# Performance work log

Hardware: AMD Instinct MI355X
Metric: run time of the kernel (lower is better)

## Reference

```python
import jax, jax.numpy as jnp
import numpy as np

M = 8          # ensemble size
B = 16384      # batch
HIST = 5       # history
L = 384        # latent_dim
A = 1          # action_dim
HID = 512      # hidden_dim
NHL = 2        # num_hidden_layers
DIN = L * HIST + A * HIST  # 1925
EPS = 1e-5     # BatchNorm eps


def setup_inputs() -> dict:
    key = jax.random.key(0)
    ks = jax.random.split(key, 6)
    w = lambda k, shape: (jax.random.normal(k, shape, jnp.float32) * 0.02)
    return {
        "z_hist": jax.random.normal(ks[0], (B, HIST, L), jnp.float32),
        "a_hist": jax.random.normal(ks[1], (B, HIST, A), jnp.float32),
        # per-model parameters, stacked along leading ensemble dim M
        "W1": w(ks[2], (M, DIN, HID)),
        "b1": jnp.zeros((M, HID), jnp.float32),
        "Wh": w(ks[3], (NHL, M, HID, HID)),
        "bh": jnp.zeros((NHL, M, HID), jnp.float32),
        "gamma": jnp.ones((NHL, M, HID), jnp.float32),
        "beta": jnp.zeros((NHL, M, HID), jnp.float32),
        "rmean": jnp.zeros((NHL, M, HID), jnp.float32),   # BN running mean (eval mode)
        "rvar": jnp.ones((NHL, M, HID), jnp.float32),      # BN running var (eval mode)
        "W3": w(ks[4], (M, HID, L)),
        "b3": jnp.zeros((M, L), jnp.float32),
    }


def reference(z_hist, a_hist, W1, b1, Wh, bh, gamma, beta, rmean, rvar, W3, b3):
    # EnsembleTransitionModel.forward, batched over the ensemble dim instead of
    # a Python loop over models. BatchNorm in eval mode; Dropout inactive (eval).
    bsz = z_hist.shape[0]
    x = jnp.concatenate([z_hist.reshape(bsz, -1), a_hist.reshape(bsz, -1)], axis=1)  # [B, DIN]
    # input projection + ReLU: [M, B, HID]
    h = jax.nn.relu(jnp.einsum('bi,mih->mbh', x, W1) + b1[:, None, :])
    n_layers = Wh.shape[0]
    for l in range(n_layers):  # small fixed structural loop (num_hidden_layers)
        h = jnp.einsum('mbh,mhk->mbk', h, Wh[l]) + bh[l][:, None, :]
        h = (h - rmean[l][:, None, :]) * jax.lax.rsqrt(rvar[l][:, None, :] + EPS)
        h = jax.nn.relu(h * gamma[l][:, None, :] + beta[l][:, None, :])
    delta = jnp.einsum('mbh,mhl->mbl', h, W3) + b3[:, None, :]
    # residual: pred_z = z_t + delta, broadcast over ensemble dim
    return delta + z_hist[:, -1, :][None, :, :]
```

## Files before the change

kernel.cpp:

```cpp
#include <hip/hip_runtime.h>
#include <hip/hip_bf16.h>

#define M_ENS 8
#define BATCH 16384
#define HIST 5
#define LDIM 384
#define HID 512
#define NHL 2
#define DIN 1925
#define KPAD 1984

typedef unsigned short u16;
typedef unsigned int u32;
typedef __attribute__((ext_vector_type(8))) short bf16x8;
typedef __attribute__((ext_vector_type(4))) float f32x4;

__device__ __forceinline__ u16 f2b(float f) {
    u32 u = __builtin_bit_cast(u32, f);
    u32 r = (u + 0x7fffu + ((u >> 16) & 1u)) >> 16;
    return (u16)r;
}

__global__ void build_x(const float* __restrict__ z, const float* __restrict__ a,
                        u16* __restrict__ xp) {
    int idx = blockIdx.x * 256 + threadIdx.x;
    int b = idx / (KPAD / 2);
    int k2 = (idx % (KPAD / 2)) * 2;
    if (b >= BATCH) return;
    u32 packed = 0;
#pragma unroll
    for (int j = 0; j < 2; ++j) {
        int k = k2 + j;
        float v = 0.f;
        if (k < HIST * LDIM) v = z[(size_t)b * (HIST * LDIM) + k];
        else if (k < DIN)    v = a[b * HIST + (k - HIST * LDIM)];
        packed |= ((u32)f2b(v)) << (16 * j);
    }
    *(u32*)(&xp[(size_t)b * KPAD + k2]) = packed;
}

__global__ void transpose_cvt(const float* __restrict__ in, u16* __restrict__ out,
                              int R, int C, int Rp) {
    __shared__ float tile[32][33];
    const float* inb = in + (size_t)blockIdx.z * R * C;
    u16* outb = out + (size_t)blockIdx.z * C * Rp;
    int r0 = blockIdx.x * 32, c0 = blockIdx.y * 32;
    int tx = threadIdx.x & 31, ty = threadIdx.x >> 5;
#pragma unroll
    for (int i = 0; i < 32; i += 8) {
        int r = r0 + ty + i;
        float v = 0.f;
        if (r < R) v = inb[(size_t)r * C + c0 + tx];
        tile[ty + i][tx] = v;
    }
    __syncthreads();
#pragma unroll
    for (int i = 0; i < 32; i += 8) {
        outb[(size_t)(c0 + ty + i) * Rp + r0 + tx] = f2b(tile[tx][ty + i]);
    }
}

__global__ void make_tables(const float* __restrict__ bh, const float* __restrict__ gamma,
                            const float* __restrict__ beta, const float* __restrict__ rmean,
                            const float* __restrict__ rvar, float* __restrict__ s,
                            float* __restrict__ t, int n) {
    int i = blockIdx.x * 256 + threadIdx.x;
    if (i >= n) return;
    float inv = rsqrtf(rvar[i] + 1e-5f);
    float sc = gamma[i] * inv;
    s[i] = sc;
    t[i] = (bh[i] - rmean[i]) * sc + beta[i];
}

template <int MODE>
__global__ __launch_bounds__(256, 2) void gemm_bt(
    const u16* __restrict__ A, size_t aStride, int lda,
    const u16* __restrict__ Bt, size_t bStride,
    const float* __restrict__ Sv, const float* __restrict__ Tv, int ptStride,
    u16* __restrict__ Ho, size_t hStride,
    float* __restrict__ Fo, size_t fStride,
    const float* __restrict__ Zres,
    int K, int m0) {
    __shared__ u16 As[128 * 64];
    __shared__ u16 Bs[128 * 64];

    const int tid = threadIdx.x;
    const int lane = tid & 63;
    const int wid = tid >> 6;
    const int wr = (wid >> 1) * 64;
    const int wc = (wid & 1) * 64;
    const int z = blockIdx.z;
    const int rowBase = blockIdx.x * 128;
    const int colBase = blockIdx.y * 128;

    const u16* Ab = A + (size_t)z * aStride;
    const u16* Bb = Bt + (size_t)z * bStride;

    f32x4 acc[4][4] = {};

    int aoff[4], boff[4];
#pragma unroll
    for (int f = 0; f < 4; ++f) {
        int ar = wr + f * 16 + (lane & 15);
        aoff[f] = (ar * 128 + ((lane >> 4) * 16)) ^ ((ar & 7) << 4);
        int br = wc + f * 16 + (lane & 15);
        boff[f] = (br * 128 + ((lane >> 4) * 16)) ^ ((br & 7) << 4);
    }

    for (int k0 = 0; k0 < K; k0 += 64) {
#pragma unroll
        for (int i = 0; i < 4; ++i) {
            int gg = i * 256 + tid;
            int row = gg >> 3, gc = gg & 7;
            const u16* srcA = Ab + (size_t)(rowBase + row) * lda + k0 + ((gc ^ (row & 7)) << 3);
            __builtin_amdgcn_global_load_lds(
                (const __attribute__((address_space(1))) void*)srcA,
                (__attribute__((address_space(3))) void*)(As + gg * 8), 16, 0, 0);
            const u16* srcB = Bb + (size_t)(colBase + row) * K + k0 + ((gc ^ (row & 7)) << 3);
            __builtin_amdgcn_global_load_lds(
                (const __attribute__((address_space(1))) void*)srcB,
                (__attribute__((address_space(3))) void*)(Bs + gg * 8), 16, 0, 0);
        }
        __syncthreads();
#pragma unroll
        for (int kk = 0; kk < 2; ++kk) {
            bf16x8 af[4], bfr[4];
#pragma unroll
            for (int f = 0; f < 4; ++f) {
                af[f]  = *(const bf16x8*)((const char*)As + (aoff[f] ^ (kk << 6)));
                bfr[f] = *(const bf16x8*)((const char*)Bs + (boff[f] ^ (kk << 6)));
            }
#pragma unroll
            for (int i = 0; i < 4; ++i)
#pragma unroll
                for (int j = 0; j < 4; ++j)
                    acc[i][j] = __builtin_amdgcn_mfma_f32_16x16x32_bf16(af[i], bfr[j], acc[i][j], 0, 0, 0);
        }
        __syncthreads();
    }

    const int mg = m0 + z;
#pragma unroll
    for (int i = 0; i < 4; ++i) {
        int rbase = rowBase + wr + i * 16 + ((lane >> 4) << 2);
#pragma unroll
        for (int j = 0; j < 4; ++j) {
            int n = colBase + wc + j * 16 + (lane & 15);
            if (MODE == 0) {
                float bias = Tv[(size_t)mg * ptStride + n];
                u16* H = Ho + (size_t)z * hStride;
#pragma unroll
                for (int q = 0; q < 4; ++q) {
                    float v = acc[i][j][q] + bias;
                    v = v > 0.f ? v : 0.f;
                    H[(size_t)(rbase + q) * HID + n] = f2b(v);
                }
            } else if (MODE == 1) {
                float sc = Sv[(size_t)mg * ptStride + n];
                float tt = Tv[(size_t)mg * ptStride + n];
                u16* H = Ho + (size_t)z * hStride;
#pragma unroll
                for (int q = 0; q < 4; ++q) {
                    float v = acc[i][j][q] * sc + tt;
                    v = v > 0.f ? v : 0.f;
                    H[(size_t)(rbase + q) * HID + n] = f2b(v);
                }
            } else {
                float bias = Tv[(size_t)mg * ptStride + n];
                float* F = Fo + (size_t)z * fStride;
#pragma unroll
                for (int q = 0; q < 4; ++q) {
                    int b = rbase + q;
                    float v = acc[i][j][q] + bias + Zres[(size_t)b * (HIST * LDIM) + (HIST - 1) * LDIM + n];
                    F[(size_t)b * LDIM + n] = v;
                }
            }
        }
    }
}

extern "C" void kernel_launch(void* const* d_in, const int* in_sizes, int n_in,
                              void* d_out, int out_size, void* d_ws, size_t ws_size,
                              hipStream_t stream) {
    const float* z_hist = (const float*)d_in[0];
    const float* a_hist = (const float*)d_in[1];
    const float* W1    = (const float*)d_in[2];
    const float* b1    = (const float*)d_in[3];
    const float* Wh    = (const float*)d_in[4];
    const float* bh    = (const float*)d_in[5];
    const float* gamma = (const float*)d_in[6];
    const float* beta  = (const float*)d_in[7];
    const float* rmean = (const float*)d_in[8];
    const float* rvar  = (const float*)d_in[9];
    const float* W3    = (const float*)d_in[10];
    const float* b3    = (const float*)d_in[11];
    float* out = (float*)d_out;

    char* ws = (char*)d_ws;
    size_t off = 0;
    auto alloc = [&](size_t bytes) {
        void* p = ws + off;
        off = (off + bytes + 255) & ~(size_t)255;
        return p;
    };
    u16* xp  = (u16*)alloc((size_t)BATCH * KPAD * 2);
    u16* W1t = (u16*)alloc((size_t)M_ENS * HID * KPAD * 2);
    u16* Wht = (u16*)alloc((size_t)NHL * M_ENS * HID * HID * 2);
    u16* W3t = (u16*)alloc((size_t)M_ENS * LDIM * HID * 2);
    float* stab = (float*)alloc((size_t)NHL * M_ENS * HID * 4);
    float* ttab = (float*)alloc((size_t)NHL * M_ENS * HID * 4);
    size_t fixed = off;
    size_t hFull = (size_t)M_ENS * BATCH * HID * 2;
    int MC = (fixed + 2 * hFull <= ws_size) ? M_ENS : 1;
    u16* h0 = (u16*)alloc((size_t)MC * BATCH * HID * 2);
    u16* h1 = (u16*)alloc((size_t)MC * BATCH * HID * 2);

    {
        int total = BATCH * KPAD / 2;
        build_x<<<(total + 255) / 256, 256, 0, stream>>>(z_hist, a_hist, xp);
        dim3 g1(KPAD / 32, HID / 32, M_ENS);
        transpose_cvt<<<g1, 256, 0, stream>>>(W1, W1t, DIN, HID, KPAD);
        dim3 g2(HID / 32, HID / 32, NHL * M_ENS);
        transpose_cvt<<<g2, 256, 0, stream>>>(Wh, Wht, HID, HID, HID);
        dim3 g3(HID / 32, LDIM / 32, M_ENS);
        transpose_cvt<<<g3, 256, 0, stream>>>(W3, W3t, HID, LDIM, HID);
        int n = NHL * M_ENS * HID;
        make_tables<<<(n + 255) / 256, 256, 0, stream>>>(bh, gamma, beta, rmean, rvar, stab, ttab, n);
    }

    for (int m0 = 0; m0 < M_ENS; m0 += MC) {
        dim3 grid(BATCH / 128, HID / 128, MC);
        gemm_bt<0><<<grid, 256, 0, stream>>>(
            xp, 0, KPAD,
            W1t + (size_t)m0 * HID * KPAD, (size_t)HID * KPAD,
            nullptr, b1, HID,
            h0, (size_t)BATCH * HID, nullptr, 0, nullptr,
            KPAD, m0);
        for (int l = 0; l < NHL; ++l) {
            u16* hin = l ? h1 : h0;
            u16* hout = l ? h0 : h1;
            gemm_bt<1><<<grid, 256, 0, stream>>>(
                hin, (size_t)BATCH * HID, HID,
                Wht + ((size_t)l * M_ENS + m0) * HID * HID, (size_t)HID * HID,
                stab + (size_t)l * M_ENS * HID, ttab + (size_t)l * M_ENS * HID, HID,
                hout, (size_t)BATCH * HID, nullptr, 0, nullptr,
                HID, m0);
        }
        dim3 gridO(BATCH / 128, LDIM / 128, MC);
        gemm_bt<2><<<gridO, 256, 0, stream>>>(
            h0, (size_t)BATCH * HID, HID,
            W3t + (size_t)m0 * LDIM * HID, (size_t)LDIM * HID,
            nullptr, b3, LDIM,
            nullptr, 0,
            out + (size_t)m0 * BATCH * LDIM, (size_t)BATCH * LDIM,
            z_hist,
            HID, m0);
    }
}
```

Before: 659.9 us.

## Add 256x256-tile pipelined MFMA GEMM for input and hidden layers

Adds a new 512-thread GEMM kernel with 256x256 output tiles. It uses double-buffered LDS staged by direct global-to-LDS loads with an XOR swizzle, interleaves quarter-tile MFMA phases with prefetch, and raises wave priority around the MFMAs. The input projection is run as one wide GEMM across all ensemble members sharing the same x tile, and blocks are remapped in a swizzled order for cache locality. K padding grows from 1984 to 2048 so the K loop is uniform, which adds some wasted work. The output layer and the low-memory fallback keep the old kernel, but the fallback now passes m0=0, which mis-indexes per-model parameters in that path.

```diff
diff --git a/kernel.cpp b/kernel.cpp
--- a/kernel.cpp
+++ b/kernel.cpp
@@ -8,7 +8,7 @@
 #define HID 512
 #define NHL 2
 #define DIN 1925
-#define KPAD 1984
+#define KP 2048
 
 typedef unsigned short u16;
 typedef unsigned int u32;
@@ -24,8 +24,8 @@
 __global__ void build_x(const float* __restrict__ z, const float* __restrict__ a,
                         u16* __restrict__ xp) {
     int idx = blockIdx.x * 256 + threadIdx.x;
-    int b = idx / (KPAD / 2);
-    int k2 = (idx % (KPAD / 2)) * 2;
+    int b = idx / (KP / 2);
+    int k2 = (idx % (KP / 2)) * 2;
     if (b >= BATCH) return;
     u32 packed = 0;
 #pragma unroll
@@ -36,7 +36,7 @@
         else if (k < DIN)    v = a[b * HIST + (k - HIST * LDIM)];
         packed |= ((u32)f2b(v)) << (16 * j);
     }
-    *(u32*)(&xp[(size_t)b * KPAD + k2]) = packed;
+    *(u32*)(&xp[(size_t)b * KP + k2]) = packed;
 }
 
 __global__ void transpose_cvt(const float* __restrict__ in, u16* __restrict__ out,
@@ -70,6 +70,184 @@
     float sc = gamma[i] * inv;
     s[i] = sc;
     t[i] = (bh[i] - rmean[i]) * sc + beta[i];
+}
+
+#define BARRIER asm volatile("s_barrier" ::: "memory")
+
+template <int MODE>
+__global__ __launch_bounds__(512, 2) void gemm8p(
+    const u16* __restrict__ A, const u16* __restrict__ Bw,
+    const float* __restrict__ Sv, const float* __restrict__ Tv,
+    u16* __restrict__ Ho, int K) {
+    extern __shared__ char smem[];
+    const int tid = threadIdx.x;
+    const int lane = tid & 63;
+    const int wid = tid >> 6;
+    const int wm = wid >> 2;
+    const int wn = wid & 3;
+
+    const int nwg = gridDim.x;
+    const int swz = (blockIdx.x & 7) * (nwg >> 3) + (blockIdx.x >> 3);
+
+    int rowT, colT, mI;
+    const u16 *Ab, *Bb;
+    int lda, ldb;
+    if (MODE == 0) {
+        rowT = swz >> 4; colT = swz & 15;
+        Ab = A; lda = KP;
+        Bb = Bw + (size_t)colT * 256 * KP; ldb = KP;
+        mI = 0;
+    } else {
+        mI = swz >> 7;
+        int rem = swz & 127;
+        rowT = rem >> 1; colT = rem & 1;
+        Ab = A + (size_t)mI * BATCH * HID; lda = HID;
+        Bb = Bw + (size_t)mI * HID * HID + (size_t)colT * 256 * HID; ldb = HID;
+    }
+    const int rowBase = rowT * 256;
+    const int NT = K >> 6;
+
+    auto STAGE = [&](int par, int op, int half, int tk) {
+#pragma unroll
+        for (int i = 0; i < 2; ++i) {
+            int ii = wid * 2 + i;
+            int row = ii * 8 + (lane >> 3);
+            int gc = lane & 7;
+            const u16* src;
+            if (op == 0)
+                src = Ab + (size_t)(rowBase + half * 128 + row) * lda + tk * 64 + ((gc ^ (row & 7)) << 3);
+            else
+                src = Bb + (size_t)(half * 128 + row) * ldb + tk * 64 + ((gc ^ (row & 7)) << 3);
+            u16* dst = (u16*)(smem + par * 65536 + op * 32768 + half * 16384) + (size_t)(ii * 64 + lane) * 8;
+            __builtin_amdgcn_global_load_lds((const __attribute__((address_space(1))) void*)src,
+                                             (__attribute__((address_space(3))) void*)dst, 16, 0, 0);
+        }
+    };
+
+    const int laneRow = lane & 15;
+    int xg[2];
+    xg[0] = (((lane >> 4)) ^ (lane & 7)) << 4;
+    xg[1] = ((4 | (lane >> 4)) ^ (lane & 7)) << 4;
+#define RDF(base, r, kk) (*(const bf16x8*)((base) + (size_t)(r) * 128 + xg[kk]))
+
+    f32x4 acc[8][4] = {};
+    bf16x8 af[4][2], bfr[4][2];
+    const int bcol0 = (wn & 1) * 64;
+
+    STAGE(0, 1, 0, 0); STAGE(0, 1, 1, 0);
+    STAGE(0, 0, 0, 0); STAGE(0, 0, 1, 0);
+    if (NT > 1) { STAGE(1, 1, 0, 1); STAGE(1, 1, 1, 1); }
+    asm volatile("s_waitcnt vmcnt(4)" ::: "memory");
+    BARRIER;
+
+    for (int T = 0; T < NT; ++T) {
+        const int p = T & 1;
+        const char* pA = smem + p * 65536 + wm * 16384;
+        const char* pB = smem + p * 65536 + 32768 + (wn >> 1) * 16384;
+
+#pragma unroll
+        for (int mf = 0; mf < 4; ++mf) {
+            af[mf][0] = RDF(pA, mf * 16 + laneRow, 0);
+            af[mf][1] = RDF(pA, mf * 16 + laneRow, 1);
+        }
+#pragma unroll
+        for (int nf = 0; nf < 2; ++nf) {
+            bfr[nf][0] = RDF(pB, bcol0 + nf * 16 + laneRow, 0);
+            bfr[nf][1] = RDF(pB, bcol0 + nf * 16 + laneRow, 1);
+        }
+        if (T + 1 < NT) STAGE((T + 1) & 1, 0, 0, T + 1);
+        BARRIER;
+        __builtin_amdgcn_s_setprio(1);
+#pragma unroll
+        for (int kk = 0; kk < 2; ++kk)
+#pragma unroll
+            for (int mf = 0; mf < 4; ++mf)
+#pragma unroll
+                for (int nf = 0; nf < 2; ++nf)
+                    acc[mf][nf] = __builtin_amdgcn_mfma_f32_16x16x32_bf16(af[mf][kk], bfr[nf][kk], acc[mf][nf], 0, 0, 0);
+        __builtin_amdgcn_s_setprio(0);
+        BARRIER;
+
+#pragma unroll
+        for (int nf = 2; nf < 4; ++nf) {
+            bfr[nf][0] = RDF(pB, bcol0 + nf * 16 + laneRow, 0);
+            bfr[nf][1] = RDF(pB, bcol0 + nf * 16 + laneRow, 1);
+        }
+        if (T + 1 < NT) STAGE((T + 1) & 1, 0, 1, T + 1);
+        BARRIER;
+        __builtin_amdgcn_s_setprio(1);
+#pragma unroll
+        for (int kk = 0; kk < 2; ++kk)
+#pragma unroll
+            for (int mf = 0; mf < 4; ++mf)
+#pragma unroll
+                for (int nf = 2; nf < 4; ++nf)
+                    acc[mf][nf] = __builtin_amdgcn_mfma_f32_16x16x32_bf16(af[mf][kk], bfr[nf][kk], acc[mf][nf], 0, 0, 0);
+        __builtin_amdgcn_s_setprio(0);
+        BARRIER;
+
+#pragma unroll
+        for (int mf = 0; mf < 4; ++mf) {
+            af[mf][0] = RDF(pA, (4 + mf) * 16 + laneRow, 0);
+            af[mf][1] = RDF(pA, (4 + mf) * 16 + laneRow, 1);
+        }
+        if (T + 2 < NT) STAGE(p, 1, 0, T + 2);
+        BARRIER;
+        __builtin_amdgcn_s_setprio(1);
+#pragma unroll
+        for (int kk = 0; kk < 2; ++kk)
+#pragma unroll
+            for (int mf = 0; mf < 4; ++mf)
+#pragma unroll
+                for (int nf = 2; nf < 4; ++nf)
+                    acc[4 + mf][nf] = __builtin_amdgcn_mfma_f32_16x16x32_bf16(af[mf][kk], bfr[nf][kk], acc[4 + mf][nf], 0, 0, 0);
+        __builtin_amdgcn_s_setprio(0);
+        BARRIER;
+
+        if (T + 2 < NT) {
+            STAGE(p, 1, 1, T + 2);
+            asm volatile("s_waitcnt vmcnt(4)" ::: "memory");
+        } else {
+            asm volatile("s_waitcnt vmcnt(0)" ::: "memory");
+        }
+        BARRIER;
+        __builtin_amdgcn_s_setprio(1);
+#pragma unroll
+        for (int kk = 0; kk < 2; ++kk)
+#pragma unroll
+            for (int mf = 0; mf < 4; ++mf)
+#pragma unroll
+                for (int nf = 0; nf < 2; ++nf)
+                    acc[4 + mf][nf] = __builtin_amdgcn_mfma_f32_16x16x32_bf16(af[mf][kk], bfr[nf][kk], acc[4 + mf][nf], 0, 0, 0);
+        __builtin_amdgcn_s_setprio(0);
+        BARRIER;
+    }
+
+#pragma unroll
+    for (int mf = 0; mf < 8; ++mf) {
+        int row = rowBase + wm * 128 + mf * 16 + ((lane >> 4) << 2);
+#pragma unroll
+        for (int nf = 0; nf < 4; ++nf) {
+            int c = colT * 256 + wn * 64 + nf * 16 + (lane & 15);
+            if (MODE == 0) {
+                float tb = Tv[c];
+                size_t base = (size_t)(c >> 9) * BATCH * HID + (c & 511);
+#pragma unroll
+                for (int q = 0; q < 4; ++q) {
+                    float v = acc[mf][nf][q] + tb;
+                    Ho[base + (size_t)(row + q) * HID] = f2b(v > 0.f ? v : 0.f);
+                }
+            } else {
+                float sc = Sv[mI * HID + c], tb = Tv[mI * HID + c];
+                u16* H = Ho + (size_t)mI * BATCH * HID;
+#pragma unroll
+                for (int q = 0; q < 4; ++q) {
+                    float v = acc[mf][nf][q] * sc + tb;
+                    H[(size_t)(row + q) * HID + c] = f2b(v > 0.f ? v : 0.f);
+                }
+            }
+        }
+    }
 }
 
 template <int MODE>
@@ -203,23 +381,24 @@
         off = (off + bytes + 255) & ~(size_t)255;
         return p;
     };
-    u16* xp  = (u16*)alloc((size_t)BATCH * KPAD * 2);
-    u16* W1t = (u16*)alloc((size_t)M_ENS * HID * KPAD * 2);
+    u16* xp  = (u16*)alloc((size_t)BATCH * KP * 2);
+    u16* W1t = (u16*)alloc((size_t)M_ENS * HID * KP * 2);
     u16* Wht = (u16*)alloc((size_t)NHL * M_ENS * HID * HID * 2);
     u16* W3t = (u16*)alloc((size_t)M_ENS * LDIM * HID * 2);
     float* stab = (float*)alloc((size_t)NHL * M_ENS * HID * 4);
     float* ttab = (float*)alloc((size_t)NHL * M_ENS * HID * 4);
     size_t fixed = off;
     size_t hFull = (size_t)M_ENS * BATCH * HID * 2;
-    int MC = (fixed + 2 * hFull <= ws_size) ? M_ENS : 1;
+    bool full = (fixed + 2 * hFull <= ws_size);
+    int MC = full ? M_ENS : 1;
     u16* h0 = (u16*)alloc((size_t)MC * BATCH * HID * 2);
     u16* h1 = (u16*)alloc((size_t)MC * BATCH * HID * 2);
 
     {
-        int total = BATCH * KPAD / 2;
+        int total = BATCH * KP / 2;
         build_x<<<(total + 255) / 256, 256, 0, stream>>>(z_hist, a_hist, xp);
-        dim3 g1(KPAD / 32, HID / 32, M_ENS);
-        transpose_cvt<<<g1, 256, 0, stream>>>(W1, W1t, DIN, HID, KPAD);
+        dim3 g1(KP / 32, HID / 32, M_ENS);
+        transpose_cvt<<<g1, 256, 0, stream>>>(W1, W1t, DIN, HID, KP);
         dim3 g2(HID / 32, HID / 32, NHL * M_ENS);
         transpose_cvt<<<g2, 256, 0, stream>>>(Wh, Wht, HID, HID, HID);
         dim3 g3(HID / 32, LDIM / 32, M_ENS);
@@ -228,32 +407,52 @@
         make_tables<<<(n + 255) / 256, 256, 0, stream>>>(bh, gamma, beta, rmean, rvar, stab, ttab, n);
     }
 
-    for (int m0 = 0; m0 < M_ENS; m0 += MC) {
-        dim3 grid(BATCH / 128, HID / 128, MC);
-        gemm_bt<0><<<grid, 256, 0, stream>>>(
-            xp, 0, KPAD,
-            W1t + (size_t)m0 * HID * KPAD, (size_t)HID * KPAD,
-            nullptr, b1, HID,
-            h0, (size_t)BATCH * HID, nullptr, 0, nullptr,
-            KPAD, m0);
-        for (int l = 0; l < NHL; ++l) {
-            u16* hin = l ? h1 : h0;
-            u16* hout = l ? h0 : h1;
-            gemm_bt<1><<<grid, 256, 0, stream>>>(
-                hin, (size_t)BATCH * HID, HID,
-                Wht + ((size_t)l * M_ENS + m0) * HID * HID, (size_t)HID * HID,
-                stab + (size_t)l * M_ENS * HID, ttab + (size_t)l * M_ENS * HID, HID,
-                hout, (size_t)BATCH * HID, nullptr, 0, nullptr,
-                HID, m0);
-        }
-        dim3 gridO(BATCH / 128, LDIM / 128, MC);
+    if (full) {
+        (void)hipFuncSetAttribute(reinterpret_cast<const void*>(&gemm8p<0>),
+                                  hipFuncAttributeMaxDynamicSharedMemorySize, 131072);
+        (void)hipFuncSetAttribute(reinterpret_cast<const void*>(&gemm8p<1>),
+                                  hipFuncAttributeMaxDynamicSharedMemorySize, 131072);
+        gemm8p<0><<<1024, 512, 131072, stream>>>(xp, W1t, nullptr, b1, h0, KP);
+        gemm8p<1><<<1024, 512, 131072, stream>>>(h0, Wht, stab, ttab, h1, HID);
+        gemm8p<1><<<1024, 512, 131072, stream>>>(h1, Wht + (size_t)M_ENS * HID * HID,
+                                                 stab + M_ENS * HID, ttab + M_ENS * HID, h0, HID);
+        dim3 gridO(BATCH / 128, LDIM / 128, M_ENS);
         gemm_bt<2><<<gridO, 256, 0, stream>>>(
             h0, (size_t)BATCH * HID, HID,
-            W3t + (size_t)m0 * LDIM * HID, (size_t)LDIM * HID,
+            W3t, (size_t)LDIM * HID,
             nullptr, b3, LDIM,
             nullptr, 0,
-            out + (size_t)m0 * BATCH * LDIM, (size_t)BATCH * LDIM,
+            out, (size_t)BATCH * LDIM,
             z_hist,
-            HID, m0);
-    }
-}
+            HID, 0);
+    } else {
+        for (int m0 = 0; m0 < M_ENS; m0 += MC) {
+            dim3 grid(BATCH / 128, HID / 128, MC);
+            gemm_bt<0><<<grid, 256, 0, stream>>>(
+                xp, 0, KP,
+                W1t + (size_t)m0 * HID * KP, (size_t)HID * KP,
+                nullptr, b1, HID,
+                h0, (size_t)BATCH * HID, nullptr, 0, nullptr,
+                KP, m0);
+            for (int l = 0; l < NHL; ++l) {
+                u16* hin = l ? h1 : h0;
+                u16* hout = l ? h0 : h1;
+                gemm_bt<1><<<grid, 256, 0, stream>>>(
+                    hin, (size_t)BATCH * HID, HID,
+                    Wht + ((size_t)l * M_ENS + m0) * HID * HID, (size_t)HID * HID,
+                    stab + (size_t)l * M_ENS * HID, ttab + (size_t)l * M_ENS * HID, HID,
+                    hout, (size_t)BATCH * HID, nullptr, 0, nullptr,
+                    HID, m0);
+            }
+            dim3 gridO(BATCH / 128, LDIM / 128, MC);
+            gemm_bt<2><<<gridO, 256, 0, stream>>>(
+                h0, (size_t)BATCH * HID, HID,
+                W3t + (size_t)m0 * LDIM * HID, (size_t)LDIM * HID,
+                nullptr, b3, LDIM,
+                nullptr, 0,
+                out + (size_t)m0 * BATCH * LDIM, (size_t)BATCH * LDIM,
+                z_hist,
+                HID, 0);
+        }
+    }
+}
```

After: 634.7 us. 3.8% less time.
